# Kernel optimization log

Measured on AMD Instinct MI355X. Metric: run time of the kernel, lower is better.

## Reference

```python
import jax, jax.numpy as jnp
import numpy as np

EPS = 1e-12

def _l2norm(x):
    return x / jnp.maximum(jnp.linalg.norm(x, axis=-1, keepdims=True), EPS)

def setup_inputs() -> dict:
    key = jax.random.key(0)
    ks = jax.random.split(key, 11)
    B, L, HID, M = 64, 512, 768, 128
    R, P, T = 64, 8, 32
    return {
        "hidden_states": jax.random.normal(ks[0], (B, L, HID), dtype=jnp.float32),
        "ctx_mask": jax.random.randint(ks[1], (B, L), 0, 2, dtype=jnp.int32),
        "between_mask": jax.random.randint(ks[2], (B, L), 0, 2, dtype=jnp.int32),
        "subj_type_id": jax.random.randint(ks[3], (B,), 0, T, dtype=jnp.int32),
        "obj_type_id": jax.random.randint(ks[4], (B,), 0, T, dtype=jnp.int32),
        "subj_first": jax.random.randint(ks[5], (B,), 0, 2, dtype=jnp.int32),
        "proj_W": jax.random.normal(ks[6], (HID, M), dtype=jnp.float32) * 0.02,
        "label_probes": jax.random.normal(ks[7], (R, P, M), dtype=jnp.float32) * 0.02,
        "subj_type_W": jax.random.normal(ks[8], (T, M), dtype=jnp.float32) * 0.02,
        "obj_type_W": jax.random.normal(ks[9], (T, M), dtype=jnp.float32) * 0.02,
        "dir_W": jax.random.normal(ks[10], (2, M), dtype=jnp.float32) * 0.02,
    }

def reference(hidden_states, ctx_mask, between_mask, subj_type_id, obj_type_id,
              subj_first, proj_W, label_probes, subj_type_W, obj_type_W, dir_W):
    # Document token embeddings: project + L2 normalize. [B, L, M]
    D = _l2norm(hidden_states @ proj_W)

    between = between_mask.astype(bool)
    ctx = ctx_mask.astype(bool)
    has_between = jnp.any(between, axis=1)  # [B]
    evidence = jnp.where(has_between[:, None], between, ctx)  # [B, L]

    # Conditioned probes: [B, R, P, M]
    Q = (label_probes[None]
         + subj_type_W[subj_type_id][:, None, None]
         + obj_type_W[obj_type_id][:, None, None]
         + dir_W[subj_first][:, None, None])
    Q = _l2norm(Q)

    # MaxSim: [B, R, P, L]
    sim = jnp.einsum('brhm,blm->brhl', Q, D)
    sim = jnp.where(evidence[:, None, None, :], sim, -10000.0)
    mx = sim.max(axis=3)                        # [B, R, P]
    mx = jnp.where(mx > -1000.0, mx, 0.0)       # zero out fully-masked probes
    logits = mx.sum(axis=2)                     # [B, R]
    return logits
```

## Files before the change

### kernel.cpp

```cpp
#include <hip/hip_runtime.h>
#include <hip/hip_bf16.h>

typedef __attribute__((ext_vector_type(8))) __bf16 bf16x8;
typedef __attribute__((ext_vector_type(4))) float f32x4;

#define B_   64
#define L_   512
#define HID_ 768
#define M_   128
#define R_   64
#define P_   8

__device__ __forceinline__ int swz(int row, int k, int stride) {
    return row * stride + (k ^ ((row & 7) << 3));
}

#define GLL16(gp, lp)                                                        \
    __builtin_amdgcn_global_load_lds(                                        \
        (const __attribute__((address_space(1))) void*)(gp),                 \
        (__attribute__((address_space(3))) void*)(lp), 16, 0, 0)

__global__ __launch_bounds__(256) void k_wt(const float* __restrict__ W,
                                            __bf16* __restrict__ Wt) {
    int idx = blockIdx.x * 256 + threadIdx.x;
    int k = idx >> 7, n = idx & 127;
    int c = k >> 6, kk = k & 63;
    Wt[c * 8192 + n * 64 + (kk ^ ((n & 7) << 3))] = (__bf16)W[idx];
}

__global__ __launch_bounds__(512, 4) void k_proj(const float* __restrict__ hidden,
                                                 const __bf16* __restrict__ Wt,
                                                 __bf16* __restrict__ D) {
    __shared__ __align__(16) __bf16 Al[2][64 * 64];
    __shared__ __align__(16) __bf16 Bl[2][128 * 64];
    __shared__ float nbuf[2][64];
    const int t = threadIdx.x;
    const int lane = t & 63, w = t >> 6;
    const int rlo = lane & 15, g = lane >> 4;
    const int rb = w & 3, ch = w >> 2;
    const int row0 = blockIdx.x * 512 + blockIdx.y * 64;

    f32x4 acc[4] = {};

    const int ar = t >> 3;
    const int ac = (t & 7) * 8;
    const float* arow = hidden + (size_t)(row0 + ar) * HID_ + ac;

    GLL16(Wt + w * 1024 + lane * 8,       &Bl[0][w * 1024]);
    GLL16(Wt + w * 1024 + 512 + lane * 8, &Bl[0][w * 1024 + 512]);
    {
        float4 f0 = *(const float4*)(arow);
        float4 f1 = *(const float4*)(arow + 4);
        bf16x8 v;
        v[0]=(__bf16)f0.x; v[1]=(__bf16)f0.y; v[2]=(__bf16)f0.z; v[3]=(__bf16)f0.w;
        v[4]=(__bf16)f1.x; v[5]=(__bf16)f1.y; v[6]=(__bf16)f1.z; v[7]=(__bf16)f1.w;
        *(bf16x8*)&Al[0][swz(ar, ac, 64)] = v;
    }
    __syncthreads();

    for (int ci = 0; ci < 12; ++ci) {
        const int cur = ci & 1;
        const bool pre = ci < 11;
        float4 f0, f1;
        if (pre) {
            const __bf16* wsrc = Wt + (ci + 1) * 8192 + w * 1024;
            GLL16(wsrc + lane * 8,       &Bl[cur ^ 1][w * 1024]);
            GLL16(wsrc + 512 + lane * 8, &Bl[cur ^ 1][w * 1024 + 512]);
            const float* src = arow + (ci + 1) * 64;
            f0 = *(const float4*)(src);
            f1 = *(const float4*)(src + 4);
        }
#pragma unroll
        for (int s = 0; s < 2; ++s) {
            int kk = s * 32 + g * 8;
            bf16x8 aF = *(const bf16x8*)&Al[cur][swz(rb * 16 + rlo, kk, 64)];
#pragma unroll
            for (int c = 0; c < 4; ++c) {
                bf16x8 bF = *(const bf16x8*)&Bl[cur][swz(ch * 64 + c * 16 + rlo, kk, 64)];
                acc[c] = __builtin_amdgcn_mfma_f32_16x16x32_bf16(aF, bF, acc[c], 0, 0, 0);
            }
        }
        if (pre) {
            bf16x8 v;
            v[0]=(__bf16)f0.x; v[1]=(__bf16)f0.y; v[2]=(__bf16)f0.z; v[3]=(__bf16)f0.w;
            v[4]=(__bf16)f1.x; v[5]=(__bf16)f1.y; v[6]=(__bf16)f1.z; v[7]=(__bf16)f1.w;
            *(bf16x8*)&Al[cur ^ 1][swz(ar, ac, 64)] = v;
        }
        __syncthreads();
    }

    float ss[4] = {0.f, 0.f, 0.f, 0.f};
#pragma unroll
    for (int c = 0; c < 4; ++c)
#pragma unroll
        for (int r = 0; r < 4; ++r) ss[r] += acc[c][r] * acc[c][r];
#pragma unroll
    for (int r = 0; r < 4; ++r)
#pragma unroll
        for (int off = 1; off < 16; off <<= 1) ss[r] += __shfl_xor(ss[r], off);
    if (rlo == 0) {
#pragma unroll
        for (int r = 0; r < 4; ++r) nbuf[ch][rb * 16 + g * 4 + r] = ss[r];
    }
    __syncthreads();
    float sc[4];
#pragma unroll
    for (int r = 0; r < 4; ++r) {
        float tot = nbuf[0][rb * 16 + g * 4 + r] + nbuf[1][rb * 16 + g * 4 + r];
        sc[r] = 1.0f / fmaxf(sqrtf(tot), 1e-12f);
    }

    __bf16* Dst = (__bf16*)Al;
#pragma unroll
    for (int c = 0; c < 4; ++c)
#pragma unroll
        for (int r = 0; r < 4; ++r) {
            int row = rb * 16 + g * 4 + r;
            int col = ch * 64 + c * 16 + rlo;
            Dst[row * 128 + (col ^ ((row & 7) << 3))] = (__bf16)(acc[c][r] * sc[r]);
        }
    __syncthreads();
#pragma unroll
    for (int h = 0; h < 2; ++h) {
        int row = (t >> 4) + h * 32;
        int seg = t & 15;
        bf16x8 v = *(const bf16x8*)&Dst[row * 128 + seg * 8];
        *(bf16x8*)(D + (size_t)(row0 + row) * M_ + seg * 8) = v;
    }
}

__global__ __launch_bounds__(256) void k_sim(const float* __restrict__ lp,
                                             const float* __restrict__ sW,
                                             const float* __restrict__ oW,
                                             const float* __restrict__ dW,
                                             const int* __restrict__ st,
                                             const int* __restrict__ ot,
                                             const int* __restrict__ sf,
                                             const int* __restrict__ ctx,
                                             const int* __restrict__ btw,
                                             const __bf16* __restrict__ D,
                                             float* __restrict__ out) {
    __shared__ __align__(16) __bf16 Dl[2][128 * 128];
    __shared__ float evl[L_];
    __shared__ int anyf;
    const int t = threadIdx.x;
    const int lane = t & 63, w = t >> 6;
    const int rlo = lane & 15, g = lane >> 4;
    const int b = blockIdx.x, pt = blockIdx.y;

    const __bf16* Db = D + (size_t)b * L_ * M_;

#pragma unroll
    for (int q = 0; q < 8; ++q)
        GLL16(Db + q * 2048 + w * 512 + lane * 8, &Dl[0][q * 2048 + w * 512]);

    if (t == 0) anyf = 0;
    __syncthreads();
    int v0 = btw[b * L_ + t], v1 = btw[b * L_ + t + 256];
    int c0 = ctx[b * L_ + t], c1 = ctx[b * L_ + t + 256];
    if (v0 | v1) anyf = 1;
    __syncthreads();
    const int any = anyf;
    evl[t]       = (any ? v0 : c0) ? 1.0f : 0.0f;
    evl[t + 256] = (any ? v1 : c1) ? 1.0f : 0.0f;

    const int sb = st[b], ob = ot[b], db = sf[b];
    const float* lpp = lp + (size_t)(pt * 64 + w * 16 + rlo) * M_;
    const float* sv  = sW + sb * M_;
    const float* ov  = oW + ob * M_;
    const float* dv  = dW + db * M_;
    float qv[32];
    float ssq = 0.f;
#pragma unroll
    for (int ks = 0; ks < 4; ++ks) {
        const int m0 = ks * 32 + g * 8;
#pragma unroll
        for (int h = 0; h < 2; ++h) {
            float4 a  = *(const float4*)(lpp + m0 + h * 4);
            float4 s4 = *(const float4*)(sv  + m0 + h * 4);
            float4 o4 = *(const float4*)(ov  + m0 + h * 4);
            float4 d4 = *(const float4*)(dv  + m0 + h * 4);
            float x0 = a.x + s4.x + o4.x + d4.x;
            float x1 = a.y + s4.y + o4.y + d4.y;
            float x2 = a.z + s4.z + o4.z + d4.z;
            float x3 = a.w + s4.w + o4.w + d4.w;
            qv[ks * 8 + h * 4 + 0] = x0;
            qv[ks * 8 + h * 4 + 1] = x1;
            qv[ks * 8 + h * 4 + 2] = x2;
            qv[ks * 8 + h * 4 + 3] = x3;
            ssq += x0 * x0 + x1 * x1 + x2 * x2 + x3 * x3;
        }
    }
    ssq += __shfl_xor(ssq, 16);
    ssq += __shfl_xor(ssq, 32);
    const float scq = 1.0f / fmaxf(sqrtf(ssq), 1e-12f);
    bf16x8 qF[4];
#pragma unroll
    for (int ks = 0; ks < 4; ++ks)
#pragma unroll
        for (int j = 0; j < 8; ++j)
            qF[ks][j] = (__bf16)(qv[ks * 8 + j] * scq);

    __syncthreads();

    float vmax[4] = {-1e30f, -1e30f, -1e30f, -1e30f};

    for (int tc = 0; tc < 4; ++tc) {
        const int cur = tc & 1;
        if (tc < 3) {
#pragma unroll
            for (int q = 0; q < 8; ++q)
                GLL16(Db + (tc + 1) * 16384 + q * 2048 + w * 512 + lane * 8,
                      &Dl[cur ^ 1][q * 2048 + w * 512]);
        }
#pragma unroll
        for (int tt = 0; tt < 8; ++tt) {
            f32x4 acc = {};
#pragma unroll
            for (int ks = 0; ks < 4; ++ks) {
                bf16x8 bF = *(const bf16x8*)&Dl[cur][swz(tt * 16 + rlo, ks * 32 + g * 8, 128)];
                acc = __builtin_amdgcn_mfma_f32_16x16x32_bf16(qF[ks], bF, acc, 0, 0, 0);
            }
            float e = evl[tc * 128 + tt * 16 + rlo];
#pragma unroll
            for (int r = 0; r < 4; ++r) {
                float sv2 = (e > 0.5f) ? acc[r] : -1e4f;
                vmax[r] = fmaxf(vmax[r], sv2);
            }
        }
        __syncthreads();
    }

#pragma unroll
    for (int r = 0; r < 4; ++r)
#pragma unroll
        for (int off = 1; off < 16; off <<= 1)
            vmax[r] = fmaxf(vmax[r], __shfl_xor(vmax[r], off));

    float psum = 0.f;
#pragma unroll
    for (int r = 0; r < 4; ++r)
        psum += (vmax[r] > -1000.0f) ? vmax[r] : 0.0f;

    float rtot = psum + __shfl_xor(psum, 16);
    if ((lane & 31) == 0) {
        int rr = pt * 8 + w * 2 + (g >> 1);
        out[b * R_ + rr] = rtot;
    }
}

extern "C" void kernel_launch(void* const* d_in, const int* in_sizes, int n_in,
                              void* d_out, int out_size, void* d_ws, size_t ws_size,
                              hipStream_t stream) {
    const float* hidden = (const float*)d_in[0];
    const int*   ctx    = (const int*)d_in[1];
    const int*   btw    = (const int*)d_in[2];
    const int*   st     = (const int*)d_in[3];
    const int*   ot     = (const int*)d_in[4];
    const int*   sf     = (const int*)d_in[5];
    const float* W      = (const float*)d_in[6];
    const float* lp     = (const float*)d_in[7];
    const float* sW     = (const float*)d_in[8];
    const float* oW     = (const float*)d_in[9];
    const float* dW     = (const float*)d_in[10];
    float* out = (float*)d_out;

    char* ws = (char*)d_ws;
    __bf16* Wt = (__bf16*)ws;
    __bf16* D  = (__bf16*)(ws + 196608);

    k_wt  <<<(HID_ * M_) / 256, 256, 0, stream>>>(W, Wt);
    k_proj<<<dim3(B_, 8), 512, 0, stream>>>(hidden, Wt, D);
    k_sim <<<dim3(B_, 8), 256, 0, stream>>>(lp, sW, oW, dW, st, ot, sf, ctx, btw, D, out);
}
```

Baseline: 44.01 us.

## Fuse projection and MaxSim into one kernel with per-chunk partial max reduction

Merges the projection GEMM and the probe similarity into a single kernel. Each 1024-thread block projects a 128-token chunk, normalises it into shared memory, and immediately computes similarities against all 512 probes. Partial maxima per chunk go to a workspace, and a small reduce kernel combines them. This removes the write and reread of the bf16 D tensor and one launch. In exchange, every block recomputes all probe vectors, uses more registers, and runs only 256 large blocks.

After: 54.48 us. +23.8%, slower.

```diff
diff --git a/kernel.cpp b/kernel.cpp
--- a/kernel.cpp
+++ b/kernel.cpp
@@ -20,6 +20,13 @@
         (const __attribute__((address_space(1))) void*)(gp),                 \
         (__attribute__((address_space(3))) void*)(lp), 16, 0, 0)
 
+__device__ __forceinline__ bf16x8 cvt8(float4 f0, float4 f1) {
+    bf16x8 v;
+    v[0]=(__bf16)f0.x; v[1]=(__bf16)f0.y; v[2]=(__bf16)f0.z; v[3]=(__bf16)f0.w;
+    v[4]=(__bf16)f1.x; v[5]=(__bf16)f1.y; v[6]=(__bf16)f1.z; v[7]=(__bf16)f1.w;
+    return v;
+}
+
 __global__ __launch_bounds__(256) void k_wt(const float* __restrict__ W,
                                             __bf16* __restrict__ Wt) {
     int idx = blockIdx.x * 256 + threadIdx.x;
@@ -28,33 +35,88 @@
     Wt[c * 8192 + n * 64 + (kk ^ ((n & 7) << 3))] = (__bf16)W[idx];
 }
 
-__global__ __launch_bounds__(512, 4) void k_proj(const float* __restrict__ hidden,
-                                                 const __bf16* __restrict__ Wt,
-                                                 __bf16* __restrict__ D) {
-    __shared__ __align__(16) __bf16 Al[2][64 * 64];
+__global__ __launch_bounds__(1024, 4) void k_main(
+        const float* __restrict__ hidden, const __bf16* __restrict__ Wt,
+        const float* __restrict__ lp, const float* __restrict__ sW,
+        const float* __restrict__ oW, const float* __restrict__ dW,
+        const int* __restrict__ st, const int* __restrict__ ot,
+        const int* __restrict__ sf, const int* __restrict__ ctx,
+        const int* __restrict__ btw, float* __restrict__ pm) {
+    __shared__ __align__(16) __bf16 Al[2][128 * 64];
     __shared__ __align__(16) __bf16 Bl[2][128 * 64];
-    __shared__ float nbuf[2][64];
+    __shared__ __align__(16) __bf16 Dl[128 * 128];
+    __shared__ float nbuf[2][128];
+    __shared__ float evl[128];
+    __shared__ int anyf;
+
     const int t = threadIdx.x;
     const int lane = t & 63, w = t >> 6;
     const int rlo = lane & 15, g = lane >> 4;
-    const int rb = w & 3, ch = w >> 2;
-    const int row0 = blockIdx.x * 512 + blockIdx.y * 64;
-
-    f32x4 acc[4] = {};
+    const int b = blockIdx.x, c = blockIdx.y;
+    const int rg = w & 7, cg = w >> 3;
+    const int row0 = b * 512 + c * 128;
+
+    if (t == 0) anyf = 0;
+    __syncthreads();
+    if (t < 512) { if (btw[b * L_ + t]) anyf = 1; }
+    __syncthreads();
+    const int any = anyf;
+    if (t < 128) {
+        int j = c * 128 + t;
+        evl[t] = ((any ? btw[b * L_ + j] : ctx[b * L_ + j]) != 0) ? 1.0f : 0.0f;
+    }
 
     const int ar = t >> 3;
     const int ac = (t & 7) * 8;
     const float* arow = hidden + (size_t)(row0 + ar) * HID_ + ac;
 
-    GLL16(Wt + w * 1024 + lane * 8,       &Bl[0][w * 1024]);
-    GLL16(Wt + w * 1024 + 512 + lane * 8, &Bl[0][w * 1024 + 512]);
+    f32x4 acc[4] = {};
+
+    GLL16(Wt + w * 512 + lane * 8, &Bl[0][w * 512]);
     {
-        float4 f0 = *(const float4*)(arow);
-        float4 f1 = *(const float4*)(arow + 4);
-        bf16x8 v;
-        v[0]=(__bf16)f0.x; v[1]=(__bf16)f0.y; v[2]=(__bf16)f0.z; v[3]=(__bf16)f0.w;
-        v[4]=(__bf16)f1.x; v[5]=(__bf16)f1.y; v[6]=(__bf16)f1.z; v[7]=(__bf16)f1.w;
-        *(bf16x8*)&Al[0][swz(ar, ac, 64)] = v;
+        float4 f0 = ((const float4*)arow)[0];
+        float4 f1 = ((const float4*)arow)[1];
+        *(bf16x8*)&Al[0][swz(ar, ac, 64)] = cvt8(f0, f1);
+    }
+
+    const int sb = st[b], ob = ot[b], db = sf[b];
+    const float* sv = sW + sb * M_;
+    const float* ov = oW + ob * M_;
+    const float* dv = dW + db * M_;
+    bf16x8 qF[2][4];
+#pragma unroll
+    for (int pt2 = 0; pt2 < 2; ++pt2) {
+        const float* lpp = lp + (size_t)(w * 32 + pt2 * 16 + rlo) * M_;
+        float qv[32];
+        float ssq = 0.f;
+#pragma unroll
+        for (int ks = 0; ks < 4; ++ks) {
+#pragma unroll
+            for (int h = 0; h < 2; ++h) {
+                const int m0 = ks * 32 + g * 8 + h * 4;
+                float4 a  = *(const float4*)(lpp + m0);
+                float4 s4 = *(const float4*)(sv + m0);
+                float4 o4 = *(const float4*)(ov + m0);
+                float4 d4 = *(const float4*)(dv + m0);
+                float x0 = a.x + s4.x + o4.x + d4.x;
+                float x1 = a.y + s4.y + o4.y + d4.y;
+                float x2 = a.z + s4.z + o4.z + d4.z;
+                float x3 = a.w + s4.w + o4.w + d4.w;
+                qv[ks * 8 + h * 4 + 0] = x0;
+                qv[ks * 8 + h * 4 + 1] = x1;
+                qv[ks * 8 + h * 4 + 2] = x2;
+                qv[ks * 8 + h * 4 + 3] = x3;
+                ssq += x0 * x0 + x1 * x1 + x2 * x2 + x3 * x3;
+            }
+        }
+        ssq += __shfl_xor(ssq, 16);
+        ssq += __shfl_xor(ssq, 32);
+        const float scq = 1.0f / fmaxf(sqrtf(ssq), 1e-12f);
+#pragma unroll
+        for (int ks = 0; ks < 4; ++ks)
+#pragma unroll
+            for (int j = 0; j < 8; ++j)
+                qF[pt2][ks][j] = (__bf16)(qv[ks * 8 + j] * scq);
     }
     __syncthreads();
 
@@ -63,190 +125,112 @@
         const bool pre = ci < 11;
         float4 f0, f1;
         if (pre) {
-            const __bf16* wsrc = Wt + (ci + 1) * 8192 + w * 1024;
-            GLL16(wsrc + lane * 8,       &Bl[cur ^ 1][w * 1024]);
-            GLL16(wsrc + 512 + lane * 8, &Bl[cur ^ 1][w * 1024 + 512]);
+            GLL16(Wt + (ci + 1) * 8192 + w * 512 + lane * 8, &Bl[cur ^ 1][w * 512]);
             const float* src = arow + (ci + 1) * 64;
-            f0 = *(const float4*)(src);
-            f1 = *(const float4*)(src + 4);
+            f0 = ((const float4*)src)[0];
+            f1 = ((const float4*)src)[1];
         }
 #pragma unroll
         for (int s = 0; s < 2; ++s) {
-            int kk = s * 32 + g * 8;
-            bf16x8 aF = *(const bf16x8*)&Al[cur][swz(rb * 16 + rlo, kk, 64)];
-#pragma unroll
-            for (int c = 0; c < 4; ++c) {
-                bf16x8 bF = *(const bf16x8*)&Bl[cur][swz(ch * 64 + c * 16 + rlo, kk, 64)];
-                acc[c] = __builtin_amdgcn_mfma_f32_16x16x32_bf16(aF, bF, acc[c], 0, 0, 0);
+            const int kk = s * 32 + g * 8;
+            bf16x8 aF = *(const bf16x8*)&Al[cur][swz(rg * 16 + rlo, kk, 64)];
+#pragma unroll
+            for (int ct = 0; ct < 4; ++ct) {
+                bf16x8 bF = *(const bf16x8*)&Bl[cur][swz(cg * 64 + ct * 16 + rlo, kk, 64)];
+                acc[ct] = __builtin_amdgcn_mfma_f32_16x16x32_bf16(aF, bF, acc[ct], 0, 0, 0);
             }
         }
         if (pre) {
-            bf16x8 v;
-            v[0]=(__bf16)f0.x; v[1]=(__bf16)f0.y; v[2]=(__bf16)f0.z; v[3]=(__bf16)f0.w;
-            v[4]=(__bf16)f1.x; v[5]=(__bf16)f1.y; v[6]=(__bf16)f1.z; v[7]=(__bf16)f1.w;
-            *(bf16x8*)&Al[cur ^ 1][swz(ar, ac, 64)] = v;
+            *(bf16x8*)&Al[cur ^ 1][swz(ar, ac, 64)] = cvt8(f0, f1);
         }
         __syncthreads();
     }
 
-    float ss[4] = {0.f, 0.f, 0.f, 0.f};
-#pragma unroll
-    for (int c = 0; c < 4; ++c)
-#pragma unroll
-        for (int r = 0; r < 4; ++r) ss[r] += acc[c][r] * acc[c][r];
+    float ss[4];
+#pragma unroll
+    for (int r = 0; r < 4; ++r)
+        ss[r] = acc[0][r] * acc[0][r] + acc[1][r] * acc[1][r]
+              + acc[2][r] * acc[2][r] + acc[3][r] * acc[3][r];
 #pragma unroll
     for (int r = 0; r < 4; ++r)
 #pragma unroll
         for (int off = 1; off < 16; off <<= 1) ss[r] += __shfl_xor(ss[r], off);
     if (rlo == 0) {
 #pragma unroll
-        for (int r = 0; r < 4; ++r) nbuf[ch][rb * 16 + g * 4 + r] = ss[r];
+        for (int r = 0; r < 4; ++r) nbuf[cg][rg * 16 + g * 4 + r] = ss[r];
     }
     __syncthreads();
     float sc[4];
 #pragma unroll
     for (int r = 0; r < 4; ++r) {
-        float tot = nbuf[0][rb * 16 + g * 4 + r] + nbuf[1][rb * 16 + g * 4 + r];
-        sc[r] = 1.0f / fmaxf(sqrtf(tot), 1e-12f);
-    }
-
-    __bf16* Dst = (__bf16*)Al;
+        const int row = rg * 16 + g * 4 + r;
+        sc[r] = 1.0f / fmaxf(sqrtf(nbuf[0][row] + nbuf[1][row]), 1e-12f);
+    }
+#pragma unroll
+    for (int ct = 0; ct < 4; ++ct)
+#pragma unroll
+        for (int r = 0; r < 4; ++r) {
+            const int row = rg * 16 + g * 4 + r;
+            const int col = cg * 64 + ct * 16 + rlo;
+            Dl[row * 128 + (col ^ ((row & 7) << 3))] = (__bf16)(acc[ct][r] * sc[r]);
+        }
+    __syncthreads();
+
+    float vmax[2][4];
+#pragma unroll
+    for (int pt2 = 0; pt2 < 2; ++pt2)
+#pragma unroll
+        for (int r = 0; r < 4; ++r) vmax[pt2][r] = -1e30f;
+
+#pragma unroll
+    for (int tt = 0; tt < 8; ++tt) {
+        f32x4 pacc[2] = {};
+#pragma unroll
+        for (int ks = 0; ks < 4; ++ks) {
+            bf16x8 bF = *(const bf16x8*)&Dl[swz(tt * 16 + rlo, ks * 32 + g * 8, 128)];
+            pacc[0] = __builtin_amdgcn_mfma_f32_16x16x32_bf16(qF[0][ks], bF, pacc[0], 0, 0, 0);
+            pacc[1] = __builtin_amdgcn_mfma_f32_16x16x32_bf16(qF[1][ks], bF, pacc[1], 0, 0, 0);
+        }
+        const float e = evl[tt * 16 + rlo];
+#pragma unroll
+        for (int pt2 = 0; pt2 < 2; ++pt2)
+#pragma unroll
+            for (int r = 0; r < 4; ++r) {
+                float sv2 = (e > 0.5f) ? pacc[pt2][r] : -1e4f;
+                vmax[pt2][r] = fmaxf(vmax[pt2][r], sv2);
+            }
+    }
+
+#pragma unroll
+    for (int pt2 = 0; pt2 < 2; ++pt2)
+#pragma unroll
+        for (int r = 0; r < 4; ++r)
+#pragma unroll
+            for (int off = 1; off < 16; off <<= 1)
+                vmax[pt2][r] = fmaxf(vmax[pt2][r], __shfl_xor(vmax[pt2][r], off));
+
+    if (rlo == 0) {
+        float* dst = pm + (size_t)(b * 4 + c) * 512 + w * 32;
+#pragma unroll
+        for (int pt2 = 0; pt2 < 2; ++pt2)
+#pragma unroll
+            for (int r = 0; r < 4; ++r)
+                dst[pt2 * 16 + g * 4 + r] = vmax[pt2][r];
+    }
+}
+
+__global__ __launch_bounds__(512) void k_reduce(const float* __restrict__ pm,
+                                                float* __restrict__ out) {
+    const int b = blockIdx.x, t = threadIdx.x;
+    float m = -1e30f;
 #pragma unroll
     for (int c = 0; c < 4; ++c)
-#pragma unroll
-        for (int r = 0; r < 4; ++r) {
-            int row = rb * 16 + g * 4 + r;
-            int col = ch * 64 + c * 16 + rlo;
-            Dst[row * 128 + (col ^ ((row & 7) << 3))] = (__bf16)(acc[c][r] * sc[r]);
-        }
-    __syncthreads();
-#pragma unroll
-    for (int h = 0; h < 2; ++h) {
-        int row = (t >> 4) + h * 32;
-        int seg = t & 15;
-        bf16x8 v = *(const bf16x8*)&Dst[row * 128 + seg * 8];
-        *(bf16x8*)(D + (size_t)(row0 + row) * M_ + seg * 8) = v;
-    }
-}
-
-__global__ __launch_bounds__(256) void k_sim(const float* __restrict__ lp,
-                                             const float* __restrict__ sW,
-                                             const float* __restrict__ oW,
-                                             const float* __restrict__ dW,
-                                             const int* __restrict__ st,
-                                             const int* __restrict__ ot,
-                                             const int* __restrict__ sf,
-                                             const int* __restrict__ ctx,
-                                             const int* __restrict__ btw,
-                                             const __bf16* __restrict__ D,
-                                             float* __restrict__ out) {
-    __shared__ __align__(16) __bf16 Dl[2][128 * 128];
-    __shared__ float evl[L_];
-    __shared__ int anyf;
-    const int t = threadIdx.x;
-    const int lane = t & 63, w = t >> 6;
-    const int rlo = lane & 15, g = lane >> 4;
-    const int b = blockIdx.x, pt = blockIdx.y;
-
-    const __bf16* Db = D + (size_t)b * L_ * M_;
-
-#pragma unroll
-    for (int q = 0; q < 8; ++q)
-        GLL16(Db + q * 2048 + w * 512 + lane * 8, &Dl[0][q * 2048 + w * 512]);
-
-    if (t == 0) anyf = 0;
-    __syncthreads();
-    int v0 = btw[b * L_ + t], v1 = btw[b * L_ + t + 256];
-    int c0 = ctx[b * L_ + t], c1 = ctx[b * L_ + t + 256];
-    if (v0 | v1) anyf = 1;
-    __syncthreads();
-    const int any = anyf;
-    evl[t]       = (any ? v0 : c0) ? 1.0f : 0.0f;
-    evl[t + 256] = (any ? v1 : c1) ? 1.0f : 0.0f;
-
-    const int sb = st[b], ob = ot[b], db = sf[b];
-    const float* lpp = lp + (size_t)(pt * 64 + w * 16 + rlo) * M_;
-    const float* sv  = sW + sb * M_;
-    const float* ov  = oW + ob * M_;
-    const float* dv  = dW + db * M_;
-    float qv[32];
-    float ssq = 0.f;
-#pragma unroll
-    for (int ks = 0; ks < 4; ++ks) {
-        const int m0 = ks * 32 + g * 8;
-#pragma unroll
-        for (int h = 0; h < 2; ++h) {
-            float4 a  = *(const float4*)(lpp + m0 + h * 4);
-            float4 s4 = *(const float4*)(sv  + m0 + h * 4);
-            float4 o4 = *(const float4*)(ov  + m0 + h * 4);
-            float4 d4 = *(const float4*)(dv  + m0 + h * 4);
-            float x0 = a.x + s4.x + o4.x + d4.x;
-            float x1 = a.y + s4.y + o4.y + d4.y;
-            float x2 = a.z + s4.z + o4.z + d4.z;
-            float x3 = a.w + s4.w + o4.w + d4.w;
-            qv[ks * 8 + h * 4 + 0] = x0;
-            qv[ks * 8 + h * 4 + 1] = x1;
-            qv[ks * 8 + h * 4 + 2] = x2;
-            qv[ks * 8 + h * 4 + 3] = x3;
-            ssq += x0 * x0 + x1 * x1 + x2 * x2 + x3 * x3;
-        }
-    }
-    ssq += __shfl_xor(ssq, 16);
-    ssq += __shfl_xor(ssq, 32);
-    const float scq = 1.0f / fmaxf(sqrtf(ssq), 1e-12f);
-    bf16x8 qF[4];
-#pragma unroll
-    for (int ks = 0; ks < 4; ++ks)
-#pragma unroll
-        for (int j = 0; j < 8; ++j)
-            qF[ks][j] = (__bf16)(qv[ks * 8 + j] * scq);
-
-    __syncthreads();
-
-    float vmax[4] = {-1e30f, -1e30f, -1e30f, -1e30f};
-
-    for (int tc = 0; tc < 4; ++tc) {
-        const int cur = tc & 1;
-        if (tc < 3) {
-#pragma unroll
-            for (int q = 0; q < 8; ++q)
-                GLL16(Db + (tc + 1) * 16384 + q * 2048 + w * 512 + lane * 8,
-                      &Dl[cur ^ 1][q * 2048 + w * 512]);
-        }
-#pragma unroll
-        for (int tt = 0; tt < 8; ++tt) {
-            f32x4 acc = {};
-#pragma unroll
-            for (int ks = 0; ks < 4; ++ks) {
-                bf16x8 bF = *(const bf16x8*)&Dl[cur][swz(tt * 16 + rlo, ks * 32 + g * 8, 128)];
-                acc = __builtin_amdgcn_mfma_f32_16x16x32_bf16(qF[ks], bF, acc, 0, 0, 0);
-            }
-            float e = evl[tc * 128 + tt * 16 + rlo];
-#pragma unroll
-            for (int r = 0; r < 4; ++r) {
-                float sv2 = (e > 0.5f) ? acc[r] : -1e4f;
-                vmax[r] = fmaxf(vmax[r], sv2);
-            }
-        }
-        __syncthreads();
-    }
-
-#pragma unroll
-    for (int r = 0; r < 4; ++r)
-#pragma unroll
-        for (int off = 1; off < 16; off <<= 1)
-            vmax[r] = fmaxf(vmax[r], __shfl_xor(vmax[r], off));
-
-    float psum = 0.f;
-#pragma unroll
-    for (int r = 0; r < 4; ++r)
-        psum += (vmax[r] > -1000.0f) ? vmax[r] : 0.0f;
-
-    float rtot = psum + __shfl_xor(psum, 16);
-    if ((lane & 31) == 0) {
-        int rr = pt * 8 + w * 2 + (g >> 1);
-        out[b * R_ + rr] = rtot;
-    }
+        m = fmaxf(m, pm[(size_t)(b * 4 + c) * 512 + t]);
+    m = (m > -1000.0f) ? m : 0.0f;
+    m += __shfl_xor(m, 1);
+    m += __shfl_xor(m, 2);
+    m += __shfl_xor(m, 4);
+    if ((t & 7) == 0) out[b * R_ + (t >> 3)] = m;
 }
 
 extern "C" void kernel_launch(void* const* d_in, const int* in_sizes, int n_in,
@@ -267,9 +251,10 @@
 
     char* ws = (char*)d_ws;
     __bf16* Wt = (__bf16*)ws;
-    __bf16* D  = (__bf16*)(ws + 196608);
-
-    k_wt  <<<(HID_ * M_) / 256, 256, 0, stream>>>(W, Wt);
-    k_proj<<<dim3(B_, 8), 512, 0, stream>>>(hidden, Wt, D);
-    k_sim <<<dim3(B_, 8), 256, 0, stream>>>(lp, sW, oW, dW, st, ot, sf, ctx, btw, D, out);
-}
+    float*  pm = (float*)(ws + 196608);
+
+    k_wt    <<<(HID_ * M_) / 256, 256, 0, stream>>>(W, Wt);
+    k_main  <<<dim3(B_, 4), 1024, 0, stream>>>(hidden, Wt, lp, sW, oW, dW,
+                                               st, ot, sf, ctx, btw, pm);
+    k_reduce<<<B_, 512, 0, stream>>>(pm, out);
+}
```

## Process two probe tiles per wave in k_sim and halve its grid

Applied to the files above, without the earlier changes.

Each wave in k_sim now builds two 16-probe query fragments and runs two MFMAs per loaded D fragment, so every LDS read of the document tile is reused twice. The grid shrinks from 8 to 4 blocks per batch, which halves how often each batch's D slice is reloaded from global memory. The D swizzle widens to 16-row XOR patterns to cut LDS bank conflicts on the 128-wide rows. The cost is higher register use and fewer blocks (256 instead of 512), which may leave some CUs underused.

Result: no change. 44.08 us (+0.1%).

```diff
diff --git a/kernel.cpp b/kernel.cpp
--- a/kernel.cpp
+++ b/kernel.cpp
@@ -14,11 +14,21 @@
 __device__ __forceinline__ int swz(int row, int k, int stride) {
     return row * stride + (k ^ ((row & 7) << 3));
 }
+__device__ __forceinline__ int swz4(int row, int k) {
+    return row * 128 + (k ^ ((row & 15) << 3));
+}
 
 #define GLL16(gp, lp)                                                        \
     __builtin_amdgcn_global_load_lds(                                        \
         (const __attribute__((address_space(1))) void*)(gp),                 \
         (__attribute__((address_space(3))) void*)(lp), 16, 0, 0)
+
+__device__ __forceinline__ bf16x8 cvt8(float4 f0, float4 f1) {
+    bf16x8 v;
+    v[0]=(__bf16)f0.x; v[1]=(__bf16)f0.y; v[2]=(__bf16)f0.z; v[3]=(__bf16)f0.w;
+    v[4]=(__bf16)f1.x; v[5]=(__bf16)f1.y; v[6]=(__bf16)f1.z; v[7]=(__bf16)f1.w;
+    return v;
+}
 
 __global__ __launch_bounds__(256) void k_wt(const float* __restrict__ W,
                                             __bf16* __restrict__ Wt) {
@@ -51,10 +61,7 @@
     {
         float4 f0 = *(const float4*)(arow);
         float4 f1 = *(const float4*)(arow + 4);
-        bf16x8 v;
-        v[0]=(__bf16)f0.x; v[1]=(__bf16)f0.y; v[2]=(__bf16)f0.z; v[3]=(__bf16)f0.w;
-        v[4]=(__bf16)f1.x; v[5]=(__bf16)f1.y; v[6]=(__bf16)f1.z; v[7]=(__bf16)f1.w;
-        *(bf16x8*)&Al[0][swz(ar, ac, 64)] = v;
+        *(bf16x8*)&Al[0][swz(ar, ac, 64)] = cvt8(f0, f1);
     }
     __syncthreads();
 
@@ -81,10 +88,7 @@
             }
         }
         if (pre) {
-            bf16x8 v;
-            v[0]=(__bf16)f0.x; v[1]=(__bf16)f0.y; v[2]=(__bf16)f0.z; v[3]=(__bf16)f0.w;
-            v[4]=(__bf16)f1.x; v[5]=(__bf16)f1.y; v[6]=(__bf16)f1.z; v[7]=(__bf16)f1.w;
-            *(bf16x8*)&Al[cur ^ 1][swz(ar, ac, 64)] = v;
+            *(bf16x8*)&Al[cur ^ 1][swz(ar, ac, 64)] = cvt8(f0, f1);
         }
         __syncthreads();
     }
@@ -117,7 +121,7 @@
         for (int r = 0; r < 4; ++r) {
             int row = rb * 16 + g * 4 + r;
             int col = ch * 64 + c * 16 + rlo;
-            Dst[row * 128 + (col ^ ((row & 7) << 3))] = (__bf16)(acc[c][r] * sc[r]);
+            Dst[swz4(row, col)] = (__bf16)(acc[c][r] * sc[r]);
         }
     __syncthreads();
 #pragma unroll
@@ -165,45 +169,52 @@
     evl[t + 256] = (any ? v1 : c1) ? 1.0f : 0.0f;
 
     const int sb = st[b], ob = ot[b], db = sf[b];
-    const float* lpp = lp + (size_t)(pt * 64 + w * 16 + rlo) * M_;
-    const float* sv  = sW + sb * M_;
-    const float* ov  = oW + ob * M_;
-    const float* dv  = dW + db * M_;
-    float qv[32];
-    float ssq = 0.f;
-#pragma unroll
-    for (int ks = 0; ks < 4; ++ks) {
-        const int m0 = ks * 32 + g * 8;
-#pragma unroll
-        for (int h = 0; h < 2; ++h) {
-            float4 a  = *(const float4*)(lpp + m0 + h * 4);
-            float4 s4 = *(const float4*)(sv  + m0 + h * 4);
-            float4 o4 = *(const float4*)(ov  + m0 + h * 4);
-            float4 d4 = *(const float4*)(dv  + m0 + h * 4);
-            float x0 = a.x + s4.x + o4.x + d4.x;
-            float x1 = a.y + s4.y + o4.y + d4.y;
-            float x2 = a.z + s4.z + o4.z + d4.z;
-            float x3 = a.w + s4.w + o4.w + d4.w;
-            qv[ks * 8 + h * 4 + 0] = x0;
-            qv[ks * 8 + h * 4 + 1] = x1;
-            qv[ks * 8 + h * 4 + 2] = x2;
-            qv[ks * 8 + h * 4 + 3] = x3;
-            ssq += x0 * x0 + x1 * x1 + x2 * x2 + x3 * x3;
-        }
-    }
-    ssq += __shfl_xor(ssq, 16);
-    ssq += __shfl_xor(ssq, 32);
-    const float scq = 1.0f / fmaxf(sqrtf(ssq), 1e-12f);
-    bf16x8 qF[4];
-#pragma unroll
-    for (int ks = 0; ks < 4; ++ks)
-#pragma unroll
-        for (int j = 0; j < 8; ++j)
-            qF[ks][j] = (__bf16)(qv[ks * 8 + j] * scq);
-
-    __syncthreads();
-
-    float vmax[4] = {-1e30f, -1e30f, -1e30f, -1e30f};
+    const float* sv = sW + sb * M_;
+    const float* ov = oW + ob * M_;
+    const float* dv = dW + db * M_;
+    bf16x8 qF[2][4];
+#pragma unroll
+    for (int pt2 = 0; pt2 < 2; ++pt2) {
+        const float* lpp = lp + (size_t)(pt * 128 + w * 32 + pt2 * 16 + rlo) * M_;
+        float qv[32];
+        float ssq = 0.f;
+#pragma unroll
+        for (int ks = 0; ks < 4; ++ks) {
+#pragma unroll
+            for (int h = 0; h < 2; ++h) {
+                const int m0 = ks * 32 + g * 8 + h * 4;
+                float4 a  = *(const float4*)(lpp + m0);
+                float4 s4 = *(const float4*)(sv + m0);
+                float4 o4 = *(const float4*)(ov + m0);
+                float4 d4 = *(const float4*)(dv + m0);
+                float x0 = a.x + s4.x + o4.x + d4.x;
+                float x1 = a.y + s4.y + o4.y + d4.y;
+                float x2 = a.z + s4.z + o4.z + d4.z;
+                float x3 = a.w + s4.w + o4.w + d4.w;
+                qv[ks * 8 + h * 4 + 0] = x0;
+                qv[ks * 8 + h * 4 + 1] = x1;
+                qv[ks * 8 + h * 4 + 2] = x2;
+                qv[ks * 8 + h * 4 + 3] = x3;
+                ssq += x0 * x0 + x1 * x1 + x2 * x2 + x3 * x3;
+            }
+        }
+        ssq += __shfl_xor(ssq, 16);
+        ssq += __shfl_xor(ssq, 32);
+        const float scq = 1.0f / fmaxf(sqrtf(ssq), 1e-12f);
+#pragma unroll
+        for (int ks = 0; ks < 4; ++ks)
+#pragma unroll
+            for (int j = 0; j < 8; ++j)
+                qF[pt2][ks][j] = (__bf16)(qv[ks * 8 + j] * scq);
+    }
+
+    __syncthreads();
+
+    float vmax[2][4];
+#pragma unroll
+    for (int pt2 = 0; pt2 < 2; ++pt2)
+#pragma unroll
+        for (int r = 0; r < 4; ++r) vmax[pt2][r] = -1e30f;
 
     for (int tc = 0; tc < 4; ++tc) {
         const int cur = tc & 1;
@@ -215,37 +226,44 @@
         }
 #pragma unroll
         for (int tt = 0; tt < 8; ++tt) {
-            f32x4 acc = {};
+            f32x4 pacc[2] = {};
 #pragma unroll
             for (int ks = 0; ks < 4; ++ks) {
-                bf16x8 bF = *(const bf16x8*)&Dl[cur][swz(tt * 16 + rlo, ks * 32 + g * 8, 128)];
-                acc = __builtin_amdgcn_mfma_f32_16x16x32_bf16(qF[ks], bF, acc, 0, 0, 0);
+                bf16x8 bF = *(const bf16x8*)&Dl[cur][swz4(tt * 16 + rlo, ks * 32 + g * 8)];
+                pacc[0] = __builtin_amdgcn_mfma_f32_16x16x32_bf16(qF[0][ks], bF, pacc[0], 0, 0, 0);
+                pacc[1] = __builtin_amdgcn_mfma_f32_16x16x32_bf16(qF[1][ks], bF, pacc[1], 0, 0, 0);
             }
-            float e = evl[tc * 128 + tt * 16 + rlo];
-#pragma unroll
-            for (int r = 0; r < 4; ++r) {
-                float sv2 = (e > 0.5f) ? acc[r] : -1e4f;
-                vmax[r] = fmaxf(vmax[r], sv2);
-            }
+            const float e = evl[tc * 128 + tt * 16 + rlo];
+#pragma unroll
+            for (int pt2 = 0; pt2 < 2; ++pt2)
+#pragma unroll
+                for (int r = 0; r < 4; ++r) {
+                    float sv2 = (e > 0.5f) ? pacc[pt2][r] : -1e4f;
+                    vmax[pt2][r] = fmaxf(vmax[pt2][r], sv2);
+                }
         }
         __syncthreads();
     }
 
 #pragma unroll
-    for (int r = 0; r < 4; ++r)
-#pragma unroll
-        for (int off = 1; off < 16; off <<= 1)
-            vmax[r] = fmaxf(vmax[r], __shfl_xor(vmax[r], off));
-
-    float psum = 0.f;
-#pragma unroll
-    for (int r = 0; r < 4; ++r)
-        psum += (vmax[r] > -1000.0f) ? vmax[r] : 0.0f;
-
-    float rtot = psum + __shfl_xor(psum, 16);
-    if ((lane & 31) == 0) {
-        int rr = pt * 8 + w * 2 + (g >> 1);
-        out[b * R_ + rr] = rtot;
+    for (int pt2 = 0; pt2 < 2; ++pt2)
+#pragma unroll
+        for (int r = 0; r < 4; ++r)
+#pragma unroll
+            for (int off = 1; off < 16; off <<= 1)
+                vmax[pt2][r] = fmaxf(vmax[pt2][r], __shfl_xor(vmax[pt2][r], off));
+
+#pragma unroll
+    for (int pt2 = 0; pt2 < 2; ++pt2) {
+        float psum = 0.f;
+#pragma unroll
+        for (int r = 0; r < 4; ++r)
+            psum += (vmax[pt2][r] > -1000.0f) ? vmax[pt2][r] : 0.0f;
+        float rtot = psum + __shfl_xor(psum, 16);
+        if ((lane & 31) == 0) {
+            int rr = pt * 16 + w * 4 + pt2 * 2 + (g >> 1);
+            out[b * R_ + rr] = rtot;
+        }
     }
 }
 
@@ -271,5 +289,5 @@
 
     k_wt  <<<(HID_ * M_) / 256, 256, 0, stream>>>(W, Wt);
     k_proj<<<dim3(B_, 8), 512, 0, stream>>>(hidden, Wt, D);
-    k_sim <<<dim3(B_, 8), 256, 0, stream>>>(lp, sW, oW, dW, st, ot, sf, ctx, btw, D, out);
-}
+    k_sim <<<dim3(B_, 4), 256, 0, stream>>>(lp, sW, oW, dW, st, ot, sf, ctx, btw, D, out);
+}
```
